# Optimization experiments

Measured on AMD Instinct MI355X. Metric: run time of the kernel, lower is better.

The kernel has to match this reference:

```python
import jax, jax.numpy as jnp
import numpy as np

N_NODES = 100000
N_EDGES = 1600000
IN = 128
HID2 = 128  # hid_size * 2
OUT = 64    # hid_size


def _sage_mean(h, src, dst, W_self, W_neigh, b, n_nodes):
    # DGL SAGEConv('mean'): fc_self(h) + fc_neigh(mean of in-neighbor feats) + bias
    msg = h[src]                                             # [E, d] gather
    msum = jax.ops.segment_sum(msg, dst, num_segments=n_nodes)
    deg = jax.ops.segment_sum(jnp.ones((src.shape[0],), h.dtype), dst,
                              num_segments=n_nodes)
    agg = msum / jnp.clip(deg, 1.0)[:, None]                 # mean, 0 for isolated
    return h @ W_self + agg @ W_neigh + b


def setup_inputs() -> dict:
    key = jax.random.key(0)
    ks = jax.random.split(key, 9)
    s = lambda fan_in: 1.0 / np.sqrt(fan_in)
    return {
        "h": jax.random.normal(ks[0], (N_NODES, IN), jnp.float32),
        "edge_src": jax.random.randint(ks[1], (N_EDGES,), 0, N_NODES, jnp.int32),
        "edge_dst": jax.random.randint(ks[2], (N_EDGES,), 0, N_NODES, jnp.int32),
        "W_self1": jax.random.uniform(ks[3], (IN, HID2), jnp.float32, -s(IN), s(IN)),
        "W_neigh1": jax.random.uniform(ks[4], (IN, HID2), jnp.float32, -s(IN), s(IN)),
        "b1": jnp.zeros((HID2,), jnp.float32),
        "W_self2": jax.random.uniform(ks[5], (HID2, OUT), jnp.float32, -s(HID2), s(HID2)),
        "W_neigh2": jax.random.uniform(ks[6], (HID2, OUT), jnp.float32, -s(HID2), s(HID2)),
        "b2": jnp.zeros((OUT,), jnp.float32),
    }


def reference(h, edge_src, edge_dst, W_self1, W_neigh1, b1, W_self2, W_neigh2, b2):
    n = h.shape[0]
    h1 = jax.nn.relu(_sage_mean(h, edge_src, edge_dst, W_self1, W_neigh1, b1, n))
    h2 = jax.nn.relu(_sage_mean(h1, edge_src, edge_dst, W_self2, W_neigh2, b2, n))
    return h2
```

## Files before the change

kernel.cpp:

```cpp
#include <hip/hip_runtime.h>


typedef __attribute__((ext_vector_type(8))) short short8;
typedef __attribute__((ext_vector_type(4))) float f32x4;
typedef __attribute__((ext_vector_type(2))) float f32x2;

__device__ __forceinline__ ushort f2bf(float f) {
  uint u = __float_as_uint(f);
  u += 0x7fffu + ((u >> 16) & 1u);
  return (ushort)(u >> 16);
}

#define GLDS(src, dst)                                                        \
  __builtin_amdgcn_global_load_lds(                                           \
      (const __attribute__((address_space(1))) void*)(src),                   \
      (__attribute__((address_space(3))) void*)(dst), 16, 0, 0)

#define FENCE() asm volatile("" ::: "memory")
#define LGKM0() asm volatile("s_waitcnt lgkmcnt(0)" ::: "memory")

__global__ __launch_bounds__(256) void k_bhist(const int* __restrict__ dst,
                                               int* __restrict__ bcnt, int E) {
  __shared__ int h[512];
  int t = threadIdx.x;
  for (int i = t; i < 512; i += 256) h[i] = 0;
  __syncthreads();
  int base = blockIdx.x * 8192;
  int end = min(base + 8192, E);
  for (int e = base + t; e < end; e += 256)
    atomicAdd(&h[((uint)dst[e]) >> 8], 1);
  __syncthreads();
  for (int i = t; i < 512; i += 256)
    if (h[i]) atomicAdd(&bcnt[i], h[i]);
}

__global__ __launch_bounds__(512) void k_bscan(const int* __restrict__ bcnt,
                                               int* __restrict__ bbase,
                                               int* __restrict__ bcur, int P, int E) {
  __shared__ int s[512];
  int t = threadIdx.x;
  int v = (t < P) ? bcnt[t] : 0;
  s[t] = v;
  __syncthreads();
  for (int off = 1; off < 512; off <<= 1) {
    int x = (t >= off) ? s[t - off] : 0;
    __syncthreads();
    s[t] += x;
    __syncthreads();
  }
  int ex = s[t] - v;
  if (t < P) {
    bbase[t] = ex;
    bcur[t] = ex;
  }
  if (t == P - 1) bbase[P] = E;
}

__global__ __launch_bounds__(256) void k_bscatter(const int* __restrict__ dst,
                                                  const int* __restrict__ src,
                                                  int* __restrict__ bcur,
                                                  uint* __restrict__ bed, int E, int P) {
  __shared__ int hist[512];
  __shared__ int incl[512];
  __shared__ int gpos[512];
  __shared__ int cur[512];
  __shared__ uint stage[8192];
  __shared__ ushort bof[8192];
  int t = threadIdx.x;
  int base = blockIdx.x * 8192;
  int cnt = min(8192, E - base);
  for (int i = t; i < 512; i += 256) hist[i] = 0;
  __syncthreads();
  for (int i = t; i < cnt; i += 256)
    atomicAdd(&hist[((uint)dst[base + i]) >> 8], 1);
  __syncthreads();
  incl[t] = hist[t];
  incl[t + 256] = hist[t + 256];
  __syncthreads();
  for (int off = 1; off < 512; off <<= 1) {
    int i0 = t, i1 = t + 256;
    int a0 = (i0 >= off) ? incl[i0 - off] : 0;
    int a1 = (i1 >= off) ? incl[i1 - off] : 0;
    __syncthreads();
    incl[i0] += a0;
    incl[i1] += a1;
    __syncthreads();
  }
  cur[t] = incl[t] - hist[t];
  cur[t + 256] = incl[t + 256] - hist[t + 256];
  for (int i = t; i < P; i += 256)
    if (hist[i]) gpos[i] = atomicAdd(&bcur[i], hist[i]);
  __syncthreads();
  for (int i = t; i < cnt; i += 256) {
    int d = dst[base + i];
    int b = ((uint)d) >> 8;
    uint val = (((uint)src[base + i]) << 8) | (uint)(d & 255);
    int slot = atomicAdd(&cur[b], 1);
    stage[slot] = val;
    bof[slot] = (ushort)b;
  }
  __syncthreads();
  for (int i = t; i < cnt; i += 256) {
    int b = bof[i];
    int ex = incl[b] - hist[b];
    bed[gpos[b] + (i - ex)] = stage[i];
  }
}

__global__ __launch_bounds__(256) void k_bcsr(const uint* __restrict__ bed,
                                              const int* __restrict__ bbase,
                                              int* __restrict__ deg,
                                              int* __restrict__ rs,
                                              int* __restrict__ col, int N) {
  __shared__ int dcnt[256];
  __shared__ int sofs[256];
  int b = blockIdx.x, t = threadIdx.x;
  int e0 = bbase[b], e1 = bbase[b + 1];
  dcnt[t] = 0;
  __syncthreads();
  for (int e = e0 + t; e < e1; e += 256) atomicAdd(&dcnt[bed[e] & 255u], 1);
  __syncthreads();
  int v0 = dcnt[t];
  sofs[t] = v0;
  __syncthreads();
  for (int off = 1; off < 256; off <<= 1) {
    int x = (t >= off) ? sofs[t - off] : 0;
    __syncthreads();
    sofs[t] += x;
    __syncthreads();
  }
  int ex = sofs[t] - v0;
  int node = (b << 8) + t;
  if (node < N) {
    deg[node] = v0;
    rs[node] = e0 + ex;
  }
  __syncthreads();
  dcnt[t] = e0 + ex;
  __syncthreads();
  for (int e = e0 + t; e < e1; e += 256) {
    uint v = bed[e];
    int pos = atomicAdd(&dcnt[v & 255u], 1);
    col[pos] = (int)(v >> 8);
  }
}

__global__ __launch_bounds__(256) void k_cast(const float* __restrict__ in,
                                              ushort* __restrict__ outb,
                                              uchar* __restrict__ out8, int n8) {
  int i = blockIdx.x * 256 + threadIdx.x;
  if (i >= n8) return;
  const float4* p = reinterpret_cast<const float4*>(in) + i * 2;
  float4 a = p[0], b = p[1];
  ushort u[8];
  u[0] = f2bf(a.x); u[1] = f2bf(a.y); u[2] = f2bf(a.z); u[3] = f2bf(a.w);
  u[4] = f2bf(b.x); u[5] = f2bf(b.y); u[6] = f2bf(b.z); u[7] = f2bf(b.w);
  *reinterpret_cast<ulonglong2*>(outb + (size_t)i * 8) =
      *reinterpret_cast<ulonglong2*>(u);
  uint2 q;
  int w0 = __builtin_amdgcn_cvt_pk_fp8_f32(a.x, a.y, 0, false);
  w0 = __builtin_amdgcn_cvt_pk_fp8_f32(a.z, a.w, w0, true);
  int w1 = __builtin_amdgcn_cvt_pk_fp8_f32(b.x, b.y, 0, false);
  w1 = __builtin_amdgcn_cvt_pk_fp8_f32(b.z, b.w, w1, true);
  q.x = (uint)w0;
  q.y = (uint)w1;
  *reinterpret_cast<uint2*>(out8 + (size_t)i * 8) = q;
}

__global__ __launch_bounds__(256) void k_prep_w(const float* __restrict__ Ws1,
                                                const float* __restrict__ Wn1,
                                                const float* __restrict__ Ws2,
                                                const float* __restrict__ Wn2,
                                                ushort* __restrict__ Wt1,
                                                ushort* __restrict__ Wt2cat) {
  int idx = blockIdx.x * 256 + threadIdx.x;
  if (idx < 128 * 256) {
    int n = idx >> 8, k = idx & 255;
    float v = (k < 128) ? Ws1[(size_t)k * 128 + n] : Wn1[(size_t)(k - 128) * 128 + n];
    Wt1[idx] = f2bf(v);
  } else if (idx < 128 * 256 + 128 * 128) {
    int j = idx - 128 * 256;
    int n = j >> 7, k = j & 127;
    float v = (n < 64) ? Wn2[(size_t)k * 64 + n] : Ws2[(size_t)k * 64 + (n - 64)];
    Wt2cat[j] = f2bf(v);
  }
}

#define ACC16(v)                                                               \
  do {                                                                         \
    f32x2 f;                                                                   \
    f = __builtin_amdgcn_cvt_pk_f32_fp8((int)(v).x, false); a[0] += f.x; a[1] += f.y;  \
    f = __builtin_amdgcn_cvt_pk_f32_fp8((int)(v).x, true);  a[2] += f.x; a[3] += f.y;  \
    f = __builtin_amdgcn_cvt_pk_f32_fp8((int)(v).y, false); a[4] += f.x; a[5] += f.y;  \
    f = __builtin_amdgcn_cvt_pk_f32_fp8((int)(v).y, true);  a[6] += f.x; a[7] += f.y;  \
    f = __builtin_amdgcn_cvt_pk_f32_fp8((int)(v).z, false); a[8] += f.x; a[9] += f.y;  \
    f = __builtin_amdgcn_cvt_pk_f32_fp8((int)(v).z, true);  a[10] += f.x; a[11] += f.y;\
    f = __builtin_amdgcn_cvt_pk_f32_fp8((int)(v).w, false); a[12] += f.x; a[13] += f.y;\
    f = __builtin_amdgcn_cvt_pk_f32_fp8((int)(v).w, true);  a[14] += f.x; a[15] += f.y;\
  } while (0)

__global__ __launch_bounds__(256) void k_agg1(const uchar* __restrict__ X8,
                                              const int* __restrict__ col,
                                              const int* __restrict__ rs,
                                              const int* __restrict__ deg,
                                              ushort* __restrict__ outb, int n) {
  int node = blockIdx.x * 32 + (threadIdx.x >> 3);
  if (node >= n) return;
  int sl = threadIdx.x & 7;
  int gbase = (threadIdx.x & 63) & ~7;
  int r0 = rs[node], d = deg[node];
  float a[16] = {};
  int j = 0;
  while (j < d) {
    int cnt = min(d - j, 8);
    int myc = (sl < cnt) ? col[r0 + j + sl] : 0;
    int jj = 0;
    for (; jj + 4 <= cnt; jj += 4) {
      int c0 = __shfl(myc, gbase + jj + 0, 64);
      int c1 = __shfl(myc, gbase + jj + 1, 64);
      int c2 = __shfl(myc, gbase + jj + 2, 64);
      int c3 = __shfl(myc, gbase + jj + 3, 64);
      uint4 v0 = *reinterpret_cast<const uint4*>(X8 + (size_t)c0 * 128 + sl * 16);
      uint4 v1 = *reinterpret_cast<const uint4*>(X8 + (size_t)c1 * 128 + sl * 16);
      uint4 v2 = *reinterpret_cast<const uint4*>(X8 + (size_t)c2 * 128 + sl * 16);
      uint4 v3 = *reinterpret_cast<const uint4*>(X8 + (size_t)c3 * 128 + sl * 16);
      { uint4 v = v0; ACC16(v); }
      { uint4 v = v1; ACC16(v); }
      { uint4 v = v2; ACC16(v); }
      { uint4 v = v3; ACC16(v); }
    }
    for (; jj < cnt; jj++) {
      int c0 = __shfl(myc, gbase + jj, 64);
      uint4 v = *reinterpret_cast<const uint4*>(X8 + (size_t)c0 * 128 + sl * 16);
      ACC16(v);
    }
    j += cnt;
  }
  float rinv = 1.0f / fmaxf((float)d, 1.0f);
  ushort o[16];
#pragma unroll
  for (int k = 0; k < 16; k++) o[k] = f2bf(a[k] * rinv);
  ulonglong2* dst = reinterpret_cast<ulonglong2*>(outb + (size_t)node * 128 + sl * 16);
  dst[0] = reinterpret_cast<ulonglong2*>(o)[0];
  dst[1] = reinterpret_cast<ulonglong2*>(o)[1];
}

__global__ __launch_bounds__(256) void k_agg_out(const uchar* __restrict__ P8,
                                                 const float* __restrict__ S,
                                                 const int* __restrict__ col,
                                                 const int* __restrict__ rs,
                                                 const int* __restrict__ deg,
                                                 float* __restrict__ out, int n) {
  int node = blockIdx.x * 64 + (threadIdx.x >> 2);
  if (node >= n) return;
  int sl = threadIdx.x & 3;
  int gbase = (threadIdx.x & 63) & ~3;
  int r0 = rs[node], d = deg[node];
  float a[16] = {};
  int j = 0;
  while (j < d) {
    int cnt = min(d - j, 4);
    int myc = (sl < cnt) ? col[r0 + j + sl] : 0;
    int jj = 0;
    for (; jj + 4 <= cnt; jj += 4) {
      int c0 = __shfl(myc, gbase + 0, 64);
      int c1 = __shfl(myc, gbase + 1, 64);
      int c2 = __shfl(myc, gbase + 2, 64);
      int c3 = __shfl(myc, gbase + 3, 64);
      uint4 v0 = *reinterpret_cast<const uint4*>(P8 + (size_t)c0 * 64 + sl * 16);
      uint4 v1 = *reinterpret_cast<const uint4*>(P8 + (size_t)c1 * 64 + sl * 16);
      uint4 v2 = *reinterpret_cast<const uint4*>(P8 + (size_t)c2 * 64 + sl * 16);
      uint4 v3 = *reinterpret_cast<const uint4*>(P8 + (size_t)c3 * 64 + sl * 16);
      { uint4 v = v0; ACC16(v); }
      { uint4 v = v1; ACC16(v); }
      { uint4 v = v2; ACC16(v); }
      { uint4 v = v3; ACC16(v); }
    }
    for (; jj < cnt; jj++) {
      int c0 = __shfl(myc, gbase + jj, 64);
      uint4 v = *reinterpret_cast<const uint4*>(P8 + (size_t)c0 * 64 + sl * 16);
      ACC16(v);
    }
    j += cnt;
  }
  float rinv = 1.0f / fmaxf((float)d, 1.0f);
  const float4* sp = reinterpret_cast<const float4*>(S + (size_t)node * 64 + sl * 16);
  float4* op = reinterpret_cast<float4*>(out + (size_t)node * 64 + sl * 16);
#pragma unroll
  for (int q = 0; q < 4; q++) {
    float4 s = sp[q];
    float4 o;
    o.x = fmaxf(a[q * 4 + 0] * rinv + s.x, 0.f);
    o.y = fmaxf(a[q * 4 + 1] * rinv + s.y, 0.f);
    o.z = fmaxf(a[q * 4 + 2] * rinv + s.z, 0.f);
    o.w = fmaxf(a[q * 4 + 3] * rinv + s.w, 0.f);
    op[q] = o;
  }
}

__global__ __launch_bounds__(512) void k_persist(const ushort* __restrict__ Xb,
                                                 const ushort* __restrict__ Gb,
                                                 const ushort* __restrict__ Wt1,
                                                 const ushort* __restrict__ Wt2,
                                                 const float* __restrict__ b1,
                                                 const float* __restrict__ b2,
                                                 uchar* __restrict__ P8,
                                                 float* __restrict__ S2,
                                                 int M, int ntiles) {
  __shared__ ushort W1s[128 * 256];
  __shared__ ushort W2s[128 * 128];
  __shared__ char Xs[64 * 256 * 2];

  const int t = threadIdx.x;
  const int lane = t & 63;
  const int w = t >> 6;
  const int wm = w >> 2, wn = w & 3;

#pragma unroll
  for (int i = 0; i < 8; i++) {
    int g = t + 512 * i;
    int row = g >> 5, kph = g & 31;
    const ushort* src = Wt1 + (size_t)row * 256 + ((kph ^ (row & 7)) << 3);
    char* dst = (char*)W1s + ((g & ~63) << 4);
    GLDS(src, dst);
  }
#pragma unroll
  for (int i = 0; i < 4; i++) {
    int g = t + 512 * i;
    int row = g >> 4, kph = g & 15;
    const ushort* src = Wt2 + (size_t)row * 128 + ((kph ^ (row & 7)) << 3);
    char* dst = (char*)W2s + ((g & ~63) << 4);
    GLDS(src, dst);
  }

  float bb1[2], bb2[2];
#pragma unroll
  for (int fn = 0; fn < 2; fn++) {
    int colg = wn * 32 + fn * 16 + (lane & 15);
    bb1[fn] = b1[colg];
    bb2[fn] = (colg >= 64) ? b2[colg - 64] : 0.f;
  }

  int tile = blockIdx.x;
  if (tile >= ntiles) return;

  uint4 xr0, xr1, xr2, xr3;
#define LOADX(tl)                                                              \
  {                                                                            \
    int g, row, kk, gm;                                                        \
    const ushort* s;                                                           \
    g = t;            row = g >> 5; kk = (g & 31) ^ (row & 7);                 \
    gm = min((tl) * 64 + row, M - 1);                                          \
    s = (kk < 16) ? Xb + (size_t)gm * 128 + kk * 8                             \
                  : Gb + (size_t)gm * 128 + (kk - 16) * 8;                     \
    xr0 = *reinterpret_cast<const uint4*>(s);                                  \
    g = t + 512;      row = g >> 5; kk = (g & 31) ^ (row & 7);                 \
    gm = min((tl) * 64 + row, M - 1);                                          \
    s = (kk < 16) ? Xb + (size_t)gm * 128 + kk * 8                             \
                  : Gb + (size_t)gm * 128 + (kk - 16) * 8;                     \
    xr1 = *reinterpret_cast<const uint4*>(s);                                  \
    g = t + 1024;     row = g >> 5; kk = (g & 31) ^ (row & 7);                 \
    gm = min((tl) * 64 + row, M - 1);                                          \
    s = (kk < 16) ? Xb + (size_t)gm * 128 + kk * 8                             \
                  : Gb + (size_t)gm * 128 + (kk - 16) * 8;                     \
    xr2 = *reinterpret_cast<const uint4*>(s);                                  \
    g = t + 1536;     row = g >> 5; kk = (g & 31) ^ (row & 7);                 \
    gm = min((tl) * 64 + row, M - 1);                                          \
    s = (kk < 16) ? Xb + (size_t)gm * 128 + kk * 8                             \
                  : Gb + (size_t)gm * 128 + (kk - 16) * 8;                     \
    xr3 = *reinterpret_cast<const uint4*>(s);                                  \
  }
#define WRITEX()                                                               \
  {                                                                            \
    *reinterpret_cast<uint4*>(Xs + (size_t)t * 16) = xr0;                      \
    *reinterpret_cast<uint4*>(Xs + (size_t)(t + 512) * 16) = xr1;              \
    *reinterpret_cast<uint4*>(Xs + (size_t)(t + 1024) * 16) = xr2;             \
    *reinterpret_cast<uint4*>(Xs + (size_t)(t + 1536) * 16) = xr3;             \
  }

  LOADX(tile);
  WRITEX();
  __syncthreads();

  while (true) {
    int next = tile + gridDim.x;
    bool more = (next < ntiles);
    if (more) LOADX(next);

    f32x4 acc[2][2] = {};
#pragma unroll
    for (int ks = 0; ks < 8; ks++) {
      int ga = ks * 4 + (lane >> 4);
      short8 af[2], bf[2];
#pragma unroll
      for (int fm = 0; fm < 2; fm++) {
        int row = wm * 32 + fm * 16 + (lane & 15);
        af[fm] = *reinterpret_cast<const short8*>(
            Xs + row * 512 + ((ga ^ (row & 7)) << 4));
      }
#pragma unroll
      for (int fn = 0; fn < 2; fn++) {
        int colr = wn * 32 + fn * 16 + (lane & 15);
        bf[fn] = *reinterpret_cast<const short8*>(
            (char*)W1s + colr * 512 + ((ga ^ (colr & 7)) << 4));
      }
#pragma unroll
      for (int fm = 0; fm < 2; fm++)
#pragma unroll
        for (int fn = 0; fn < 2; fn++)
          acc[fm][fn] = __builtin_amdgcn_mfma_f32_16x16x32_bf16(
              af[fm], bf[fn], acc[fm][fn], 0, 0, 0);
    }

    __builtin_amdgcn_s_barrier();
    FENCE();

#pragma unroll
    for (int fn = 0; fn < 2; fn++) {
      int colg = wn * 32 + fn * 16 + (lane & 15);
      int gg = colg >> 3, cb = (colg & 7) * 2;
#pragma unroll
      for (int fm = 0; fm < 2; fm++) {
#pragma unroll
        for (int r = 0; r < 4; r++) {
          int rowl = wm * 32 + fm * 16 + (lane >> 4) * 4 + r;
          ushort hv = f2bf(fmaxf(acc[fm][fn][r] + bb1[fn], 0.f));
          *reinterpret_cast<ushort*>(
              Xs + rowl * 256 + ((gg ^ (rowl & 7)) << 4) + cb) = hv;
        }
      }
    }
    LGKM0();
    __builtin_amdgcn_s_barrier();
    FENCE();

    f32x4 acc2[2][2] = {};
#pragma unroll
    for (int ks = 0; ks < 4; ks++) {
      int gk = ks * 4 + (lane >> 4);
      short8 af[2], bf[2];
#pragma unroll
      for (int fm = 0; fm < 2; fm++) {
        int row = wm * 32 + fm * 16 + (lane & 15);
        af[fm] = *reinterpret_cast<const short8*>(
            Xs + row * 256 + ((gk ^ (row & 7)) << 4));
      }
#pragma unroll
      for (int fn = 0; fn < 2; fn++) {
        int colr = wn * 32 + fn * 16 + (lane & 15);
        bf[fn] = *reinterpret_cast<const short8*>(
            (char*)W2s + colr * 256 + ((gk ^ (colr & 7)) << 4));
      }
#pragma unroll
      for (int fm = 0; fm < 2; fm++)
#pragma unroll
        for (int fn = 0; fn < 2; fn++)
          acc2[fm][fn] = __builtin_amdgcn_mfma_f32_16x16x32_bf16(
              af[fm], bf[fn], acc2[fm][fn], 0, 0, 0);
    }

#pragma unroll
    for (int fn = 0; fn < 2; fn++) {
      int colg = wn * 32 + fn * 16 + (lane & 15);
#pragma unroll
      for (int fm = 0; fm < 2; fm++) {
#pragma unroll
        for (int r = 0; r < 4; r++) {
          int rowg = tile * 64 + wm * 32 + fm * 16 + (lane >> 4) * 4 + r;
          if (rowg >= M) continue;
          if (colg < 64) {
            float v = acc2[fm][fn][r];
            int b8 = __builtin_amdgcn_cvt_pk_fp8_f32(v, v, 0, false);
            P8[(size_t)rowg * 64 + colg] = (uchar)(b8 & 0xff);
          } else {
            S2[(size_t)rowg * 64 + (colg - 64)] = acc2[fm][fn][r] + bb2[fn];
          }
        }
      }
    }

    if (!more) break;
    __builtin_amdgcn_s_barrier();
    FENCE();
    WRITEX();
    LGKM0();
    __builtin_amdgcn_s_barrier();
    FENCE();
    tile = next;
  }
#undef LOADX
#undef WRITEX
}

extern "C" void kernel_launch(void* const* d_in, const int* in_sizes, int n_in,
                              void* d_out, int out_size, void* d_ws, size_t ws_size,
                              hipStream_t stream) {
  const float* h = (const float*)d_in[0];
  const int* esrc = (const int*)d_in[1];
  const int* edst = (const int*)d_in[2];
  const float* Ws1 = (const float*)d_in[3];
  const float* Wn1 = (const float*)d_in[4];
  const float* b1 = (const float*)d_in[5];
  const float* Ws2 = (const float*)d_in[6];
  const float* Wn2 = (const float*)d_in[7];
  const float* b2 = (const float*)d_in[8];
  float* out = (float*)d_out;

  const int N = in_sizes[0] / 128;
  const int E = in_sizes[1];
  const int P = (N + 255) >> 8;

  char* base = (char*)d_ws;
  size_t off = 0;
  auto alloc = [&](size_t bytes) {
    size_t o = off;
    off += (bytes + 255) & ~(size_t)255;
    return o;
  };
  int* deg = (int*)(base + alloc((size_t)N * 4));
  int* rs = (int*)(base + alloc((size_t)N * 4));
  int* bcnt = (int*)(base + alloc(513 * 4));
  int* bbase = (int*)(base + alloc(513 * 4));
  int* bcur = (int*)(base + alloc(513 * 4));
  uint* bed = (uint*)(base + alloc((size_t)E * 4));
  int* col = (int*)(base + alloc((size_t)E * 4));
  ushort* hb = (ushort*)(base + alloc((size_t)N * 128 * 2));
  uchar* h8 = (uchar*)(base + alloc((size_t)N * 128));
  ushort* aggb = (ushort*)(base + alloc((size_t)N * 128 * 2));
  ushort* Wt1 = (ushort*)(base + alloc(128 * 256 * 2));
  ushort* Wt2cat = (ushort*)(base + alloc(128 * 128 * 2));
  uchar* p8 = (uchar*)bed;
  float* s2f = (float*)aggb;

  const int NCH = (E + 8191) / 8192;
  const int NT = (N + 63) / 64;

  (void)hipMemsetAsync(bcnt, 0, 513 * 4, stream);
  k_bhist<<<NCH, 256, 0, stream>>>(edst, bcnt, E);
  k_bscan<<<1, 512, 0, stream>>>(bcnt, bbase, bcur, P, E);
  k_bscatter<<<NCH, 256, 0, stream>>>(edst, esrc, bcur, bed, E, P);
  k_bcsr<<<P, 256, 0, stream>>>(bed, bbase, deg, rs, col, N);

  k_prep_w<<<((128 * 256 + 128 * 128) + 255) / 256, 256, 0, stream>>>(
      Ws1, Wn1, Ws2, Wn2, Wt1, Wt2cat);
  k_cast<<<((N * 128 / 8) + 255) / 256, 256, 0, stream>>>(h, hb, h8, N * 128 / 8);

  k_agg1<<<(N + 31) / 32, 256, 0, stream>>>(h8, col, rs, deg, aggb, N);
  k_persist<<<256, 512, 0, stream>>>(hb, aggb, Wt1, Wt2cat, b1, b2, p8, s2f, N, NT);
  k_agg_out<<<(N + 63) / 64, 256, 0, stream>>>(p8, s2f, col, rs, deg, out, N);
}
```

Measured before the change: 182.6 us.

## Sort nodes by degree for aggregation and prefetch next column-index chunk

Builds a degree histogram inside the CSR kernel, scans it and writes a node permutation bucketed by in-degree. Both aggregation kernels then process nodes in that order so lanes within a wavefront get similar degrees, reducing divergence and idle lanes. The kernels also load the next chunk of column indices before processing the current one, to hide index-load latency. The cost is two extra small launches, a memset and an extra indirection per node; output writes are no longer coalesced across nodes in a block.

```diff
diff --git a/kernel.cpp b/kernel.cpp
--- a/kernel.cpp
+++ b/kernel.cpp
@@ -111,7 +111,8 @@
                                               const int* __restrict__ bbase,
                                               int* __restrict__ deg,
                                               int* __restrict__ rs,
-                                              int* __restrict__ col, int N) {
+                                              int* __restrict__ col,
+                                              int* __restrict__ dh, int N) {
   __shared__ int dcnt[256];
   __shared__ int sofs[256];
   int b = blockIdx.x, t = threadIdx.x;
@@ -134,6 +135,7 @@
   if (node < N) {
     deg[node] = v0;
     rs[node] = e0 + ex;
+    atomicAdd(&dh[min(v0, 255)], 1);
   }
   __syncthreads();
   dcnt[t] = e0 + ex;
@@ -143,6 +145,32 @@
     int pos = atomicAdd(&dcnt[v & 255u], 1);
     col[pos] = (int)(v >> 8);
   }
+}
+
+__global__ __launch_bounds__(256) void k_dscan(const int* __restrict__ dh,
+                                               int* __restrict__ dcur) {
+  __shared__ int s[256];
+  int t = threadIdx.x;
+  int v = dh[t];
+  s[t] = v;
+  __syncthreads();
+  for (int off = 1; off < 256; off <<= 1) {
+    int x = (t >= off) ? s[t - off] : 0;
+    __syncthreads();
+    s[t] += x;
+    __syncthreads();
+  }
+  dcur[t] = s[t] - v;
+}
+
+__global__ __launch_bounds__(256) void k_dperm(const int* __restrict__ deg,
+                                               int* __restrict__ dcur,
+                                               int* __restrict__ perm, int N) {
+  int node = blockIdx.x * 256 + threadIdx.x;
+  if (node >= N) return;
+  int b = min(deg[node], 255);
+  int pos = atomicAdd(&dcur[b], 1);
+  perm[pos] = node;
 }
 
 __global__ __launch_bounds__(256) void k_cast(const float* __restrict__ in,
@@ -203,17 +231,22 @@
                                               const int* __restrict__ col,
                                               const int* __restrict__ rs,
                                               const int* __restrict__ deg,
+                                              const int* __restrict__ perm,
                                               ushort* __restrict__ outb, int n) {
-  int node = blockIdx.x * 32 + (threadIdx.x >> 3);
-  if (node >= n) return;
+  int gid = blockIdx.x * 32 + (threadIdx.x >> 3);
+  if (gid >= n) return;
+  int node = perm[gid];
   int sl = threadIdx.x & 7;
   int gbase = (threadIdx.x & 63) & ~7;
   int r0 = rs[node], d = deg[node];
   float a[16] = {};
   int j = 0;
+  int myc = (sl < min(d, 8)) ? col[r0 + sl] : 0;
   while (j < d) {
     int cnt = min(d - j, 8);
-    int myc = (sl < cnt) ? col[r0 + j + sl] : 0;
+    int nj = j + cnt;
+    int ncnt = min(d - nj, 8);
+    int nmyc = (sl < ncnt) ? col[r0 + nj + sl] : 0;
     int jj = 0;
     for (; jj + 4 <= cnt; jj += 4) {
       int c0 = __shfl(myc, gbase + jj + 0, 64);
@@ -234,7 +267,8 @@
       uint4 v = *reinterpret_cast<const uint4*>(X8 + (size_t)c0 * 128 + sl * 16);
       ACC16(v);
     }
-    j += cnt;
+    myc = nmyc;
+    j = nj;
   }
   float rinv = 1.0f / fmaxf((float)d, 1.0f);
   ushort o[16];
@@ -250,17 +284,22 @@
                                                  const int* __restrict__ col,
                                                  const int* __restrict__ rs,
                                                  const int* __restrict__ deg,
+                                                 const int* __restrict__ perm,
                                                  float* __restrict__ out, int n) {
-  int node = blockIdx.x * 64 + (threadIdx.x >> 2);
-  if (node >= n) return;
+  int gid = blockIdx.x * 64 + (threadIdx.x >> 2);
+  if (gid >= n) return;
+  int node = perm[gid];
   int sl = threadIdx.x & 3;
   int gbase = (threadIdx.x & 63) & ~3;
   int r0 = rs[node], d = deg[node];
   float a[16] = {};
   int j = 0;
+  int myc = (sl < min(d, 4)) ? col[r0 + sl] : 0;
   while (j < d) {
     int cnt = min(d - j, 4);
-    int myc = (sl < cnt) ? col[r0 + j + sl] : 0;
+    int nj = j + cnt;
+    int ncnt = min(d - nj, 4);
+    int nmyc = (sl < ncnt) ? col[r0 + nj + sl] : 0;
     int jj = 0;
     for (; jj + 4 <= cnt; jj += 4) {
       int c0 = __shfl(myc, gbase + 0, 64);
@@ -281,7 +320,8 @@
       uint4 v = *reinterpret_cast<const uint4*>(P8 + (size_t)c0 * 64 + sl * 16);
       ACC16(v);
     }
-    j += cnt;
+    myc = nmyc;
+    j = nj;
   }
   float rinv = 1.0f / fmaxf((float)d, 1.0f);
   const float4* sp = reinterpret_cast<const float4*>(S + (size_t)node * 64 + sl * 16);
@@ -519,9 +559,12 @@
   };
   int* deg = (int*)(base + alloc((size_t)N * 4));
   int* rs = (int*)(base + alloc((size_t)N * 4));
+  int* perm = (int*)(base + alloc((size_t)N * 4));
   int* bcnt = (int*)(base + alloc(513 * 4));
   int* bbase = (int*)(base + alloc(513 * 4));
   int* bcur = (int*)(base + alloc(513 * 4));
+  int* dh = (int*)(base + alloc(256 * 4));
+  int* dcur = (int*)(base + alloc(256 * 4));
   uint* bed = (uint*)(base + alloc((size_t)E * 4));
   int* col = (int*)(base + alloc((size_t)E * 4));
   ushort* hb = (ushort*)(base + alloc((size_t)N * 128 * 2));
@@ -536,16 +579,19 @@
   const int NT = (N + 63) / 64;
 
   (void)hipMemsetAsync(bcnt, 0, 513 * 4, stream);
+  (void)hipMemsetAsync(dh, 0, 256 * 4, stream);
   k_bhist<<<NCH, 256, 0, stream>>>(edst, bcnt, E);
   k_bscan<<<1, 512, 0, stream>>>(bcnt, bbase, bcur, P, E);
   k_bscatter<<<NCH, 256, 0, stream>>>(edst, esrc, bcur, bed, E, P);
-  k_bcsr<<<P, 256, 0, stream>>>(bed, bbase, deg, rs, col, N);
+  k_bcsr<<<P, 256, 0, stream>>>(bed, bbase, deg, rs, col, dh, N);
+  k_dscan<<<1, 256, 0, stream>>>(dh, dcur);
+  k_dperm<<<(N + 255) / 256, 256, 0, stream>>>(deg, dcur, perm, N);
 
   k_prep_w<<<((128 * 256 + 128 * 128) + 255) / 256, 256, 0, stream>>>(
       Ws1, Wn1, Ws2, Wn2, Wt1, Wt2cat);
   k_cast<<<((N * 128 / 8) + 255) / 256, 256, 0, stream>>>(h, hb, h8, N * 128 / 8);
 
-  k_agg1<<<(N + 31) / 32, 256, 0, stream>>>(h8, col, rs, deg, aggb, N);
+  k_agg1<<<(N + 31) / 32, 256, 0, stream>>>(h8, col, rs, deg, perm, aggb, N);
   k_persist<<<256, 512, 0, stream>>>(hb, aggb, Wt1, Wt2cat, b1, b2, p8, s2f, N, NT);
-  k_agg_out<<<(N + 63) / 64, 256, 0, stream>>>(p8, s2f, col, rs, deg, out, N);
-}
+  k_agg_out<<<(N + 63) / 64, 256, 0, stream>>>(p8, s2f, col, rs, deg, perm, out, N);
+}
```

After: 698.4 us. 282% more time.
